# Optimization experiments

Hardware: AMD Instinct MI355X
Metric: run time of the kernel (lower is better)

## Reference

```python
import jax, jax.numpy as jnp
import numpy as np

B, E, WIN, DX, DZ, RAW = 2048, 32, 10, 14, 14, 22

def _leaky(x):
    return jnp.where(x >= 0, x, 0.01 * x)

def setup_inputs():
    key = jax.random.key(0)
    ks = jax.random.split(key, 20)
    def w(k, i, o):
        return jax.random.normal(k, (i, o), dtype=jnp.float32) / np.float32(np.sqrt(i))
    def b(k, o):
        return jax.random.normal(k, (o,), dtype=jnp.float32) * 0.01
    return {
        "raw_obs": jax.random.normal(ks[0], (B, WIN, 1, RAW), dtype=jnp.float32),
        "state_prev": jax.random.normal(ks[1], (B, E, WIN, DX), dtype=jnp.float32),
        "pm_w1": w(ks[2], WIN * DX, 256), "pm_b1": b(ks[3], 256),
        "pm_w3": w(ks[4], 256, 512), "pm_b3": b(ks[5], 512),
        "pm_wm2": w(ks[6], 512, DX), "pm_bm2": b(ks[7], DX),
        "sm_w2": w(ks[8], WIN * RAW, 256), "sm_b2": b(ks[9], 256),
        "sm_w3": w(ks[10], 256, 256), "sm_b3": b(ks[11], 256),
        "sm_w5": w(ks[12], 256, 64), "sm_b5": b(ks[13], 64),
        "sm_w6": w(ks[14], 64, DZ), "sm_b6": b(ks[15], DZ),
        "on_w1": w(ks[16], DZ, 32), "on_b1": b(ks[17], 32),
        "on_w2": w(ks[18], 32, DZ), "on_b2": b(ks[19], DZ),
    }

def reference(raw_obs, state_prev, pm_w1, pm_b1, pm_w3, pm_b3, pm_wm2, pm_bm2,
              sm_w2, sm_b2, sm_w3, sm_b3, sm_w5, sm_b5, sm_w6, sm_b6,
              on_w1, on_b1, on_w2, on_b2):
    bs, ens, win, dx = state_prev.shape
    dz = sm_w6.shape[1]
    # --- process model (LinearFlipout evaluated at mean weights) ---
    x = state_prev.reshape(bs * ens, win * dx)
    x = _leaky(x @ pm_w1 + pm_b1)
    x = _leaky(x @ pm_w3 + pm_b3)
    state_pred = (x @ pm_wm2 + pm_bm2).reshape(bs, ens, dx)   # [B,E,dx]
    state_m = state_pred.mean(axis=1)                          # [B,dx]
    A = state_pred - state_m[:, None, :]                       # [B,E,dx]
    # --- sensor model: torch repeat(E,1,1,1) tiles ensemble-major, the final
    # reshape reinterprets as batch-major; replicate that layout faithfully ---
    s = jnp.tile(raw_obs, (ens, 1, 1, 1)).reshape(bs * ens, win * raw_obs.shape[-1])
    s = _leaky(s @ sm_w2 + sm_b2)
    s = _leaky(s @ sm_w3 + sm_b3)
    s = _leaky(s @ sm_w5 + sm_b5)
    s = s @ sm_w6 + sm_b6
    ensemble_z = s.reshape(bs, ens, dz)                        # [B,E,dz]
    z = ensemble_z.mean(axis=1, keepdims=True)                 # [B,1,dz]
    # --- observation noise R = diag_embed(square(mlp(z)+c) + init) ---
    r = jax.nn.relu(z @ on_w1 + on_b1) @ on_w2 + on_b2
    r = jnp.square(r + 0.001) + 0.038729833
    R = r.reshape(bs, dz)[:, :, None] * jnp.eye(dz, dtype=r.dtype)  # [B,dz,dz]
    # --- EnKF correction ---
    S = jnp.einsum('bei,bej->bij', A, A)                       # AT @ A, [B,dx,dx]
    innovation = S / (ens - 1) + R
    K = (S / (ens - 1)) @ jnp.linalg.inv(innovation)           # [B,dx,dz]
    diff = ensemble_z - state_pred                             # (y - H_XT)^T, [B,E,dz]
    gain = jnp.einsum('bij,bej->bei', K, diff)                 # [B,E,dx]
    state_corrected = state_pred + gain
    return (state_corrected,
            state_corrected.mean(axis=1, keepdims=True),
            state_m[:, None, :],
            z,
            ensemble_z)
```

## Files before the change

kernel.cpp:

```cpp
#include <hip/hip_runtime.h>
#include <hip/hip_bf16.h>

typedef unsigned short u16;
typedef __attribute__((ext_vector_type(8))) short short8;
typedef __attribute__((ext_vector_type(4))) float floatx4;

#define MFMA_BF16 __builtin_amdgcn_mfma_f32_16x16x32_bf16

__device__ __forceinline__ u16 f2bf(float f) {
    union { __hip_bfloat16 h; u16 u; } cv;
    cv.h = __float2bfloat16(f);
    return cv.u;
}
__device__ __forceinline__ float leaky(float x) { return x >= 0.f ? x : 0.01f * x; }

#define H1S 264
#define RS 232
#define XS 168
#define H3S 72

#define O1 917504
#define O2 946176
#define O3 974848
#define O4 1003520

#define PW1   0
#define PW3   40960
#define PWM2  172032
#define PSW2  180224
#define PSW3  237568
#define PSW5  303104
#define PSW6  319488
#define PTOTAL 320512
#define WS_NEEDED 641024
#define WS_BIG (641024 + 3670016)

struct PackSeg { const float* W; int K, N, S, base, count; };
struct PackArgs { PackSeg seg[7]; };

__global__ __launch_bounds__(256) void pack_all(PackArgs pa, u16* __restrict__ P) {
    int u = blockIdx.x * 256 + threadIdx.x;
    if (u >= PTOTAL) return;
#pragma unroll
    for (int i = 0; i < 7; i++) {
        if (u >= pa.seg[i].base && u < pa.seg[i].base + pa.seg[i].count) {
            int v = u - pa.seg[i].base;
            int j = v & 7;
            int l = (v >> 3) & 63;
            int ts = v >> 9;
            int s = ts % pa.seg[i].S;
            int t = ts / pa.seg[i].S;
            int k = s * 32 + (l >> 4) * 8 + j;
            int n = t * 16 + (l & 15);
            P[u] = (k < pa.seg[i].K && n < pa.seg[i].N)
                       ? f2bf(pa.seg[i].W[k * pa.seg[i].N + n]) : (u16)0;
            return;
        }
    }
}

__global__ __launch_bounds__(512, 4) void merged_mlp(
    const float* __restrict__ Rg, const float* __restrict__ Xg,
    const u16* __restrict__ Pk,
    const float* __restrict__ b1, const float* __restrict__ b3,
    const float* __restrict__ bm2,
    const float* __restrict__ b2, const float* __restrict__ sb3,
    const float* __restrict__ b5, const float* __restrict__ b6,
    float* __restrict__ ez_out,
    float* __restrict__ sp_ws)
{
    __shared__ __align__(16) u16 ldsH[64 * H1S];
    __shared__ __align__(16) u16 ldsC[64 * H1S];

    const int tid  = threadIdx.x;
    const int lane = tid & 63;
    const int wave = tid >> 6;
    const int q    = lane >> 4;
    const int n16  = lane & 15;

    if (blockIdx.x < 32) {
        const u16* w2p = Pk + PSW2;
        const u16* w3p = Pk + PSW3;
        const u16* w5p = Pk + PSW5;
        const u16* w6p = Pk + PSW6;
        const int row0 = blockIdx.x * 64;

        for (int idx = tid; idx < 64 * 56; idx += 512) {
            int r = idx / 56, c4 = idx - r * 56;
            float4 v = {0.f, 0.f, 0.f, 0.f};
            if (c4 < 55) v = *(const float4*)&Rg[(row0 + r) * 220 + c4 * 4];
            ushort4 pk;
            pk.x = f2bf(v.x); pk.y = f2bf(v.y); pk.z = f2bf(v.z); pk.w = f2bf(v.w);
            *(ushort4*)&ldsH[r * RS + c4 * 4] = pk;
        }
        __syncthreads();

        {
            floatx4 zero = {0.f, 0.f, 0.f, 0.f};
            floatx4 acc1[4][2];
#pragma unroll
            for (int rt = 0; rt < 4; rt++)
#pragma unroll
                for (int ct = 0; ct < 2; ct++) acc1[rt][ct] = zero;
#pragma unroll
            for (int s = 0; s < 7; s++) {
                short8 a[4];
#pragma unroll
                for (int rt = 0; rt < 4; rt++)
                    a[rt] = *(const short8*)&ldsH[(rt * 16 + n16) * RS + s * 32 + q * 8];
#pragma unroll
                for (int ct = 0; ct < 2; ct++) {
                    int t = wave * 2 + ct;
                    short8 bf = *(const short8*)&w2p[((t * 7 + s) * 64 + lane) * 8];
#pragma unroll
                    for (int rt = 0; rt < 4; rt++)
                        acc1[rt][ct] = MFMA_BF16(a[rt], bf, acc1[rt][ct], 0, 0, 0);
                }
            }
#pragma unroll
            for (int ct = 0; ct < 2; ct++) {
                int col = (wave * 2 + ct) * 16 + n16;
                float bias = b2[col];
#pragma unroll
                for (int rt = 0; rt < 4; rt++)
#pragma unroll
                    for (int r = 0; r < 4; r++)
                        ldsC[(rt * 16 + q * 4 + r) * H1S + col] = f2bf(leaky(acc1[rt][ct][r] + bias));
            }
        }
        __syncthreads();

        {
            floatx4 zero = {0.f, 0.f, 0.f, 0.f};
            floatx4 acc[4][2];
#pragma unroll
            for (int rt = 0; rt < 4; rt++)
#pragma unroll
                for (int ct = 0; ct < 2; ct++) acc[rt][ct] = zero;
#pragma unroll
            for (int s = 0; s < 8; s++) {
                short8 a[4];
#pragma unroll
                for (int rt = 0; rt < 4; rt++)
                    a[rt] = *(const short8*)&ldsC[(rt * 16 + n16) * H1S + s * 32 + q * 8];
#pragma unroll
                for (int ct = 0; ct < 2; ct++) {
                    int t = wave * 2 + ct;
                    short8 bf = *(const short8*)&w3p[((t * 8 + s) * 64 + lane) * 8];
#pragma unroll
                    for (int rt = 0; rt < 4; rt++)
                        acc[rt][ct] = MFMA_BF16(a[rt], bf, acc[rt][ct], 0, 0, 0);
                }
            }
#pragma unroll
            for (int ct = 0; ct < 2; ct++) {
                int cl = (wave * 2 + ct) * 16 + n16;
                float bias = sb3[cl];
#pragma unroll
                for (int rt = 0; rt < 4; rt++)
#pragma unroll
                    for (int r = 0; r < 4; r++)
                        ldsH[(rt * 16 + q * 4 + r) * H1S + cl] = f2bf(leaky(acc[rt][ct][r] + bias));
            }
        }
        __syncthreads();

        {
            floatx4 zero = {0.f, 0.f, 0.f, 0.f};
            floatx4 acc5[4];
#pragma unroll
            for (int rt = 0; rt < 4; rt++) acc5[rt] = zero;
            int t5 = wave >> 1, sh = wave & 1;
#pragma unroll
            for (int u = 0; u < 4; u++) {
                int s = sh * 4 + u;
                short8 bf = *(const short8*)&w5p[((t5 * 8 + s) * 64 + lane) * 8];
#pragma unroll
                for (int rt = 0; rt < 4; rt++) {
                    short8 a = *(const short8*)&ldsH[(rt * 16 + n16) * H1S + s * 32 + q * 8];
                    acc5[rt] = MFMA_BF16(a, bf, acc5[rt], 0, 0, 0);
                }
            }
            float* pacc = (float*)ldsC;
#pragma unroll
            for (int rt = 0; rt < 4; rt++)
#pragma unroll
                for (int r = 0; r < 4; r++)
                    pacc[(sh * 64 + rt * 16 + q * 4 + r) * 64 + t5 * 16 + n16] = acc5[rt][r];
        }
        __syncthreads();

        {
            const float* pacc = (const float*)ldsC;
            for (int idx = tid; idx < 4096; idx += 512) {
                int row = idx >> 6, col = idx & 63;
                float v = pacc[row * 64 + col] + pacc[(64 + row) * 64 + col];
                ldsH[row * H3S + col] = f2bf(leaky(v + b5[col]));
            }
        }
        __syncthreads();

        {
            floatx4 zero = {0.f, 0.f, 0.f, 0.f};
            floatx4 acc = zero;
            int s = wave & 1, rq = wave >> 1;
            short8 bf = *(const short8*)&w6p[(s * 64 + lane) * 8];
            short8 a = *(const short8*)&ldsH[(rq * 16 + n16) * H3S + s * 32 + q * 8];
            acc = MFMA_BF16(a, bf, acc, 0, 0, 0);
            float* pacc2 = (float*)ldsC;
#pragma unroll
            for (int r = 0; r < 4; r++)
                pacc2[(s * 64 + rq * 16 + q * 4 + r) * 16 + n16] = acc[r];
        }
        __syncthreads();
        {
            const float* pacc2 = (const float*)ldsC;
            for (int idx = tid; idx < 1024; idx += 512) {
                int r = idx >> 4, c = idx & 15;
                float v = pacc2[idx] + pacc2[1024 + idx];
                if (c < 14) ez_out[(row0 + r) * 14 + c] = v + b6[c];
            }
        }
    } else {
        const u16* w1p  = Pk + PW1;
        const u16* w3p  = Pk + PW3;
        const u16* wm2p = Pk + PWM2;
        const int bb   = blockIdx.x - 32;
        const int row0 = bb * 64;

        for (int idx = tid; idx < 64 * 42; idx += 512) {
            int r = idx / 42, c4 = idx - r * 42;
            float4 v = {0.f, 0.f, 0.f, 0.f};
            if (c4 < 35) v = *(const float4*)&Xg[(row0 + r) * 140 + c4 * 4];
            ushort4 pk;
            pk.x = f2bf(v.x); pk.y = f2bf(v.y); pk.z = f2bf(v.z); pk.w = f2bf(v.w);
            *(ushort4*)&ldsH[r * XS + c4 * 4] = pk;
        }
        __syncthreads();

        {
            floatx4 zero = {0.f, 0.f, 0.f, 0.f};
            floatx4 acc1[4][2];
#pragma unroll
            for (int rt = 0; rt < 4; rt++)
#pragma unroll
                for (int ct = 0; ct < 2; ct++) acc1[rt][ct] = zero;
#pragma unroll
            for (int s = 0; s < 5; s++) {
                short8 a[4];
#pragma unroll
                for (int rt = 0; rt < 4; rt++)
                    a[rt] = *(const short8*)&ldsH[(rt * 16 + n16) * XS + s * 32 + q * 8];
#pragma unroll
                for (int ct = 0; ct < 2; ct++) {
                    int t = wave * 2 + ct;
                    short8 bf = *(const short8*)&w1p[((t * 5 + s) * 64 + lane) * 8];
#pragma unroll
                    for (int rt = 0; rt < 4; rt++)
                        acc1[rt][ct] = MFMA_BF16(a[rt], bf, acc1[rt][ct], 0, 0, 0);
                }
            }
#pragma unroll
            for (int ct = 0; ct < 2; ct++) {
                int col = (wave * 2 + ct) * 16 + n16;
                float bias = b1[col];
#pragma unroll
                for (int rt = 0; rt < 4; rt++)
#pragma unroll
                    for (int r = 0; r < 4; r++)
                        ldsC[(rt * 16 + q * 4 + r) * H1S + col] = f2bf(leaky(acc1[rt][ct][r] + bias));
            }
        }
        __syncthreads();

        floatx4 acc3[2];
        {
            floatx4 zero = {0.f, 0.f, 0.f, 0.f};
            acc3[0] = zero; acc3[1] = zero;
        }
        const int h = wave >> 2;
        const int pg = wave & 3;
#pragma unroll
        for (int c = 0; c < 2; c++) {
            floatx4 zero = {0.f, 0.f, 0.f, 0.f};
            floatx4 acc[4][2];
#pragma unroll
            for (int rt = 0; rt < 4; rt++)
#pragma unroll
                for (int ct = 0; ct < 2; ct++) acc[rt][ct] = zero;
#pragma unroll
            for (int s = 0; s < 8; s++) {
                short8 a[4];
#pragma unroll
                for (int rt = 0; rt < 4; rt++)
                    a[rt] = *(const short8*)&ldsC[(rt * 16 + n16) * H1S + s * 32 + q * 8];
#pragma unroll
                for (int ct = 0; ct < 2; ct++) {
                    int tg = c * 16 + wave * 2 + ct;
                    short8 bf = *(const short8*)&w3p[((tg * 8 + s) * 64 + lane) * 8];
#pragma unroll
                    for (int rt = 0; rt < 4; rt++)
                        acc[rt][ct] = MFMA_BF16(a[rt], bf, acc[rt][ct], 0, 0, 0);
                }
            }
#pragma unroll
            for (int ct = 0; ct < 2; ct++) {
                int cl = (wave * 2 + ct) * 16 + n16;
                float bias = b3[c * 256 + cl];
#pragma unroll
                for (int rt = 0; rt < 4; rt++)
#pragma unroll
                    for (int r = 0; r < 4; r++)
                        ldsH[(rt * 16 + q * 4 + r) * H1S + cl] = f2bf(leaky(acc[rt][ct][r] + bias));
            }
            __syncthreads();
#pragma unroll
            for (int uu = 0; uu < 2; uu++) {
                int sgl = pg * 2 + uu;
                short8 bf = *(const short8*)&wm2p[((c * 8 + sgl) * 64 + lane) * 8];
#pragma unroll
                for (int rt = 0; rt < 2; rt++) {
                    short8 a = *(const short8*)&ldsH[(h * 32 + rt * 16 + n16) * H1S + sgl * 32 + q * 8];
                    acc3[rt] = MFMA_BF16(a, bf, acc3[rt], 0, 0, 0);
                }
            }
            __syncthreads();
        }

        {
            float* pacc = (float*)ldsH;
#pragma unroll
            for (int rt = 0; rt < 2; rt++)
#pragma unroll
                for (int r = 0; r < 4; r++)
                    pacc[(pg * 64 + h * 32 + rt * 16 + q * 4 + r) * 16 + n16] = acc3[rt][r];
        }
        __syncthreads();
        {
            const float* pacc = (const float*)ldsH;
            for (int idx = tid; idx < 1024; idx += 512) {
                int r = idx >> 4, c = idx & 15;
                float v = pacc[idx] + pacc[1024 + idx] + pacc[2048 + idx] + pacc[3072 + idx];
                if (c < 14) sp_ws[(row0 + r) * 14 + c] = v + bm2[c];
            }
        }
    }
}

__global__ __launch_bounds__(256) void enkf_tail(
    const float* __restrict__ sp_all,
    const float* __restrict__ on_w1, const float* __restrict__ on_b1,
    const float* __restrict__ on_w2, const float* __restrict__ on_b2,
    float* out)
{
    __shared__ float spv[32][14];
    __shared__ float ezv[32][14];
    __shared__ float smv[14], zzv[14], rrv[14];
    __shared__ float M[14][14];
    __shared__ float G[14][28];
    __shared__ float Kmat[14][14];
    __shared__ float fac[14];
    __shared__ float hbuf[32];

    const int tid = threadIdx.x;
    const int b = blockIdx.x;

    for (int idx = tid; idx < 448; idx += 256) ((float*)spv)[idx] = sp_all[b * 448 + idx];
    {
        const float* ezsrc = out + O4 + (b & 63) * 448;
        for (int idx = tid; idx < 448; idx += 256) ((float*)ezv)[idx] = ezsrc[idx];
    }
    __syncthreads();

    if (tid < 14) {
        float s = 0.f;
        for (int e = 0; e < 32; e++) s += spv[e][tid];
        smv[tid] = s * (1.f / 32.f);
    } else if (tid >= 32 && tid < 46) {
        int c = tid - 32;
        float s = 0.f;
        for (int e = 0; e < 32; e++) s += ezv[e][c];
        zzv[c] = s * (1.f / 32.f);
    }
    __syncthreads();

    if (tid < 196) {
        int i = tid / 14, j = tid - i * 14;
        float mi = smv[i], mj = smv[j];
        float s = 0.f;
        for (int e = 0; e < 32; e++) s += (spv[e][i] - mi) * (spv[e][j] - mj);
        M[i][j] = s * (1.f / 31.f);
    } else if (tid >= 224) {
        int l = tid - 224;
        float t = on_b1[l];
        for (int k = 0; k < 14; k++) t += zzv[k] * on_w1[k * 32 + l];
        hbuf[l] = t > 0.f ? t : 0.f;
    }
    __syncthreads();

    if (tid < 14) {
        float t = on_b2[tid];
        for (int k = 0; k < 32; k++) t += hbuf[k] * on_w2[k * 14 + tid];
        t += 0.001f;
        rrv[tid] = t * t + 0.038729833f;
    }
    __syncthreads();

    for (int idx = tid; idx < 392; idx += 256) {
        int i = idx / 28, j = idx - i * 28;
        G[i][j] = (j < 14) ? (M[i][j] + (i == j ? rrv[i] : 0.f))
                           : ((j - 14 == i) ? 1.f : 0.f);
    }
    __syncthreads();

    for (int c = 0; c < 14; c++) {
        if (tid < 64) {
            float pinv = 1.f / G[c][c];
            if (tid < 28) G[c][tid] *= pinv;
            if (tid < 14 && tid != c) fac[tid] = G[tid][c];
        }
        __syncthreads();
        for (int idx = tid; idx < 392; idx += 256) {
            int i = idx / 28, j = idx - i * 28;
            if (i != c) G[i][j] -= fac[i] * G[c][j];
        }
        __syncthreads();
    }

    if (tid < 196) {
        int i = tid / 14, j = tid - i * 14;
        float s = 0.f;
        for (int k = 0; k < 14; k++) s += M[i][k] * G[k][14 + j];
        Kmat[i][j] = s;
    }
    __syncthreads();

    for (int idx = tid; idx < 448; idx += 256) {
        int e = idx / 14, i = idx - e * 14;
        float g = 0.f;
        for (int j = 0; j < 14; j++) g += Kmat[i][j] * (ezv[e][j] - spv[e][j]);
        out[b * 448 + idx] = spv[e][i] + g;
        out[O4 + b * 448 + idx] = ezv[e][i];
    }
    if (tid < 14) {
        float g = 0.f;
        for (int j = 0; j < 14; j++) g += Kmat[tid][j] * (zzv[j] - smv[j]);
        out[O1 + b * 14 + tid] = smv[tid] + g;
        out[O2 + b * 14 + tid] = smv[tid];
        out[O3 + b * 14 + tid] = zzv[tid];
    }
}

extern "C" void kernel_launch(void* const* d_in, const int* in_sizes, int n_in,
                              void* d_out, int out_size, void* d_ws, size_t ws_size,
                              hipStream_t stream) {
    (void)in_sizes; (void)n_in; (void)out_size; (void)ws_size;

    const float* raw_obs    = (const float*)d_in[0];
    const float* state_prev = (const float*)d_in[1];
    const float* pm_w1  = (const float*)d_in[2];
    const float* pm_b1  = (const float*)d_in[3];
    const float* pm_w3  = (const float*)d_in[4];
    const float* pm_b3  = (const float*)d_in[5];
    const float* pm_wm2 = (const float*)d_in[6];
    const float* pm_bm2 = (const float*)d_in[7];
    const float* sm_w2  = (const float*)d_in[8];
    const float* sm_b2  = (const float*)d_in[9];
    const float* sm_w3  = (const float*)d_in[10];
    const float* sm_b3  = (const float*)d_in[11];
    const float* sm_w5  = (const float*)d_in[12];
    const float* sm_b5  = (const float*)d_in[13];
    const float* sm_w6  = (const float*)d_in[14];
    const float* sm_b6  = (const float*)d_in[15];
    const float* on_w1  = (const float*)d_in[16];
    const float* on_b1  = (const float*)d_in[17];
    const float* on_w2  = (const float*)d_in[18];
    const float* on_b2  = (const float*)d_in[19];

    float* out = (float*)d_out;
    u16* P = (u16*)d_ws;
    float* sp_ws = (float*)((char*)d_ws + WS_NEEDED);

    PackArgs pa;
    pa.seg[0] = { pm_w1,  140, 256, 5,  PW1,  40960  };
    pa.seg[1] = { pm_w3,  256, 512, 8,  PW3,  131072 };
    pa.seg[2] = { pm_wm2, 512, 14,  16, PWM2, 8192   };
    pa.seg[3] = { sm_w2,  220, 256, 7,  PSW2, 57344  };
    pa.seg[4] = { sm_w3,  256, 256, 8,  PSW3, 65536  };
    pa.seg[5] = { sm_w5,  256, 64,  8,  PSW5, 16384  };
    pa.seg[6] = { sm_w6,  64,  14,  2,  PSW6, 1024   };
    pack_all<<<(PTOTAL + 255) / 256, 256, 0, stream>>>(pa, P);

    merged_mlp<<<1056, 512, 0, stream>>>(raw_obs, state_prev, P,
                                         pm_b1, pm_b3, pm_bm2,
                                         sm_b2, sm_b3, sm_b5, sm_b6,
                                         out + O4, sp_ws);
    enkf_tail<<<2048, 256, 0, stream>>>(sp_ws, on_w1, on_b1, on_w2, on_b2, out);
}
```

Before: 168.2 us.

## Map one batch per wavefront in EnKF tail and use the I - R·inv gain form

The EnKF tail kernel now processes four batch elements per block, one per 64-lane wavefront. All __syncthreads barriers are removed, relying on lockstep execution within a wavefront for LDS visibility. The gain uses the identity S(S+R)^-1 = I - R(S+R)^-1, which drops the separate covariance and K matrices and the extra 14x14 matmul. In exchange there is less parallelism per batch and a reliance on implicit intra-wave ordering of LDS accesses, which the compiler does not guarantee.

```diff
diff --git a/kernel.cpp b/kernel.cpp
--- a/kernel.cpp
+++ b/kernel.cpp
@@ -353,101 +353,89 @@
     const float* __restrict__ on_w2, const float* __restrict__ on_b2,
     float* out)
 {
-    __shared__ float spv[32][14];
-    __shared__ float ezv[32][14];
-    __shared__ float smv[14], zzv[14], rrv[14];
-    __shared__ float M[14][14];
-    __shared__ float G[14][28];
-    __shared__ float Kmat[14][14];
-    __shared__ float fac[14];
-    __shared__ float hbuf[32];
+    __shared__ float spv[4][32][14];
+    __shared__ float ezv[4][32][14];
+    __shared__ float smv[4][14], zzv[4][14], rrv[4][14];
+    __shared__ float G[4][14][28];
+    __shared__ float fac[4][14];
+    __shared__ float hbuf[4][32];
 
     const int tid = threadIdx.x;
-    const int b = blockIdx.x;
-
-    for (int idx = tid; idx < 448; idx += 256) ((float*)spv)[idx] = sp_all[b * 448 + idx];
+    const int w = tid >> 6;
+    const int l = tid & 63;
+    const int b = blockIdx.x * 4 + w;
+
+    float* sp = &spv[w][0][0];
+    float* ez = &ezv[w][0][0];
+
+    for (int idx = l; idx < 448; idx += 64) sp[idx] = sp_all[b * 448 + idx];
     {
         const float* ezsrc = out + O4 + (b & 63) * 448;
-        for (int idx = tid; idx < 448; idx += 256) ((float*)ezv)[idx] = ezsrc[idx];
-    }
-    __syncthreads();
-
-    if (tid < 14) {
+        for (int idx = l; idx < 448; idx += 64) ez[idx] = ezsrc[idx];
+    }
+
+    if (l < 14) {
         float s = 0.f;
-        for (int e = 0; e < 32; e++) s += spv[e][tid];
-        smv[tid] = s * (1.f / 32.f);
-    } else if (tid >= 32 && tid < 46) {
-        int c = tid - 32;
+        for (int e = 0; e < 32; e++) s += spv[w][e][l];
+        smv[w][l] = s * (1.f / 32.f);
+    } else if (l >= 32 && l < 46) {
+        int c = l - 32;
         float s = 0.f;
-        for (int e = 0; e < 32; e++) s += ezv[e][c];
-        zzv[c] = s * (1.f / 32.f);
-    }
-    __syncthreads();
-
-    if (tid < 196) {
-        int i = tid / 14, j = tid - i * 14;
-        float mi = smv[i], mj = smv[j];
+        for (int e = 0; e < 32; e++) s += ezv[w][e][c];
+        zzv[w][c] = s * (1.f / 32.f);
+    }
+
+    if (l < 32) {
+        float t = on_b1[l];
+        for (int k = 0; k < 14; k++) t += zzv[w][k] * on_w1[k * 32 + l];
+        hbuf[w][l] = t > 0.f ? t : 0.f;
+    }
+    if (l < 14) {
+        float t = on_b2[l];
+        for (int k = 0; k < 32; k++) t += hbuf[w][k] * on_w2[k * 14 + l];
+        t += 0.001f;
+        rrv[w][l] = t * t + 0.038729833f;
+    }
+
+    for (int idx = l; idx < 196; idx += 64) {
+        int i = idx / 14, j = idx - i * 14;
+        float mi = smv[w][i], mj = smv[w][j];
         float s = 0.f;
-        for (int e = 0; e < 32; e++) s += (spv[e][i] - mi) * (spv[e][j] - mj);
-        M[i][j] = s * (1.f / 31.f);
-    } else if (tid >= 224) {
-        int l = tid - 224;
-        float t = on_b1[l];
-        for (int k = 0; k < 14; k++) t += zzv[k] * on_w1[k * 32 + l];
-        hbuf[l] = t > 0.f ? t : 0.f;
-    }
-    __syncthreads();
-
-    if (tid < 14) {
-        float t = on_b2[tid];
-        for (int k = 0; k < 32; k++) t += hbuf[k] * on_w2[k * 14 + tid];
-        t += 0.001f;
-        rrv[tid] = t * t + 0.038729833f;
-    }
-    __syncthreads();
-
-    for (int idx = tid; idx < 392; idx += 256) {
-        int i = idx / 28, j = idx - i * 28;
-        G[i][j] = (j < 14) ? (M[i][j] + (i == j ? rrv[i] : 0.f))
-                           : ((j - 14 == i) ? 1.f : 0.f);
-    }
-    __syncthreads();
+        for (int e = 0; e < 32; e++) s += (spv[w][e][i] - mi) * (spv[w][e][j] - mj);
+        s *= (1.f / 31.f);
+        G[w][i][j] = s + (i == j ? rrv[w][i] : 0.f);
+        G[w][i][14 + j] = (i == j) ? 1.f : 0.f;
+    }
 
     for (int c = 0; c < 14; c++) {
-        if (tid < 64) {
-            float pinv = 1.f / G[c][c];
-            if (tid < 28) G[c][tid] *= pinv;
-            if (tid < 14 && tid != c) fac[tid] = G[tid][c];
-        }
-        __syncthreads();
-        for (int idx = tid; idx < 392; idx += 256) {
+        float pinv = 1.f / G[w][c][c];
+        if (l < 28) G[w][c][l] *= pinv;
+        if (l < 14 && l != c) fac[w][l] = G[w][l][c];
+        for (int idx = l; idx < 392; idx += 64) {
             int i = idx / 28, j = idx - i * 28;
-            if (i != c) G[i][j] -= fac[i] * G[c][j];
-        }
-        __syncthreads();
-    }
-
-    if (tid < 196) {
-        int i = tid / 14, j = tid - i * 14;
-        float s = 0.f;
-        for (int k = 0; k < 14; k++) s += M[i][k] * G[k][14 + j];
-        Kmat[i][j] = s;
-    }
-    __syncthreads();
-
-    for (int idx = tid; idx < 448; idx += 256) {
+            if (i != c) G[w][i][j] -= fac[w][i] * G[w][c][j];
+        }
+    }
+
+    for (int idx = l; idx < 448; idx += 64) {
         int e = idx / 14, i = idx - e * 14;
-        float g = 0.f;
-        for (int j = 0; j < 14; j++) g += Kmat[i][j] * (ezv[e][j] - spv[e][j]);
-        out[b * 448 + idx] = spv[e][i] + g;
-        out[O4 + b * 448 + idx] = ezv[e][i];
-    }
-    if (tid < 14) {
-        float g = 0.f;
-        for (int j = 0; j < 14; j++) g += Kmat[tid][j] * (zzv[j] - smv[j]);
-        out[O1 + b * 14 + tid] = smv[tid] + g;
-        out[O2 + b * 14 + tid] = smv[tid];
-        out[O3 + b * 14 + tid] = zzv[tid];
+        float acc = 0.f;
+        for (int j = 0; j < 14; j++)
+            acc += G[w][i][14 + j] * (ezv[w][e][j] - spv[w][e][j]);
+        float di = ezv[w][e][i] - spv[w][e][i];
+        float g = di - rrv[w][i] * acc;
+        out[b * 448 + idx] = spv[w][e][i] + g;
+        out[O4 + b * 448 + idx] = ezv[w][e][i];
+    }
+    if (l < 14) {
+        float acc = 0.f;
+        for (int j = 0; j < 14; j++)
+            acc += G[w][l][14 + j] * (zzv[w][j] - smv[w][j]);
+        float di = zzv[w][l] - smv[w][l];
+        float g = di - rrv[w][l] * acc;
+        out[O1 + b * 14 + l] = smv[w][l] + g;
+        out[O2 + b * 14 + l] = smv[w][l];
+        out[O3 + b * 14 + l] = zzv[w][l];
     }
 }
 
@@ -495,5 +483,5 @@
                                          pm_b1, pm_b3, pm_bm2,
                                          sm_b2, sm_b3, sm_b5, sm_b6,
                                          out + O4, sp_ws);
-    enkf_tail<<<2048, 256, 0, stream>>>(sp_ws, on_w1, on_b1, on_w2, on_b2, out);
+    enkf_tail<<<512, 256, 0, stream>>>(sp_ws, on_w1, on_b1, on_w2, on_b2, out);
 }
```

After: 174.1 us. +3.5%, slower.
